# Kernel tuning notes

Measured on AMD Instinct MI355X. Metric: run time of the kernel, lower is better.

## Reference

```python
import jax, jax.numpy as jnp
import numpy as np

D = 1024
N = 4096
K = 16


def setup_inputs() -> dict:
    key = jax.random.key(0)
    ks = jax.random.split(key, 10)
    s = 1.0 / np.sqrt(3 * D)
    return {
        "token": jax.random.normal(ks[0], (N, D), jnp.float32),
        "routed_tokens": jax.random.normal(ks[1], (N, K, D), jnp.float32),
        "sim_row": jax.random.normal(ks[2], (N, K), jnp.float32),
        "delta_emb": jax.random.normal(ks[3], (N, K, D), jnp.float32),
        "W_logic": jax.random.uniform(ks[4], (3 * D, D), jnp.float32, -s, s),
        "b_logic": jax.random.uniform(ks[5], (D,), jnp.float32, -s, s),
        "ln_gamma": jnp.ones((D,), jnp.float32),
        "ln_beta": jnp.zeros((D,), jnp.float32),
        "W_gate": jax.random.uniform(ks[6], (3 * D, D), jnp.float32, -s, s),
        "b_gate": jax.random.uniform(ks[7], (D,), jnp.float32, -s, s),
    }


def _layernorm(x, gamma, beta, eps=1e-5):
    mu = jnp.mean(x, axis=-1, keepdims=True)
    var = jnp.mean(jnp.square(x - mu), axis=-1, keepdims=True)
    return (x - mu) * jax.lax.rsqrt(var + eps) * gamma + beta


def reference(token, routed_tokens, sim_row, delta_emb,
              W_logic, b_logic, ln_gamma, ln_beta, W_gate, b_gate):
    n, k, d = routed_tokens.shape
    token_exp = jnp.broadcast_to(token[:, None, :], (n, k, d))
    combined = jnp.concatenate([token_exp, routed_tokens, delta_emb], axis=-1)  # [N,K,3D]
    h = jnp.einsum('nke,ed->nkd', combined, W_logic) + b_logic
    fused = _layernorm(jax.nn.gelu(h, approximate=False), ln_gamma, ln_beta)  # [N,K,D]
    sim_w = jax.nn.softmax(sim_row, axis=-1)  # [N,K]
    arg_summary = jnp.einsum('nk,nkd->nd', sim_w, fused)  # [N,D]
    gate_in = jnp.concatenate([token, arg_summary, arg_summary], axis=-1)  # [N,3D]
    gate = jax.nn.sigmoid(gate_in @ W_gate + b_gate)  # [N,D]
    return (arg_summary, gate)
```

## Files before the change

### kernel.cpp

```cpp
#include <hip/hip_runtime.h>
#include <hip/hip_bf16.h>


typedef __attribute__((ext_vector_type(4))) float f32x4;
typedef __attribute__((ext_vector_type(8))) short bf16x8;

__device__ __forceinline__ ushort f2bf(float f) {
  unsigned b = __builtin_bit_cast(unsigned, f);
  b += 0x7FFFu + ((b >> 16) & 1u);
  return (ushort)(b >> 16);
}
__device__ __forceinline__ unsigned pk2(float a, float b) {
  return (unsigned)f2bf(a) | ((unsigned)f2bf(b) << 16);
}

__device__ __forceinline__ unsigned swz(unsigned a) {
  return a ^ (((a >> 7) & 3u) << 4);
}

__device__ __forceinline__ bf16x8 cvt8(const float* p) {
  f32x4 a = *(const f32x4*)p;
  f32x4 b = *(const f32x4*)(p + 4);
  bf16x8 r;
  r[0] = (short)f2bf(a[0]); r[1] = (short)f2bf(a[1]);
  r[2] = (short)f2bf(a[2]); r[3] = (short)f2bf(a[3]);
  r[4] = (short)f2bf(b[0]); r[5] = (short)f2bf(b[1]);
  r[6] = (short)f2bf(b[2]); r[7] = (short)f2bf(b[3]);
  return r;
}

__global__ __launch_bounds__(256) void prep_kernel(
    const float* __restrict__ Wl, const float* __restrict__ Wg,
    ushort* __restrict__ Bmain, ushort* __restrict__ Bk1,
    ushort* __restrict__ Bgate) {
  __shared__ float L[32][129];
  int t = threadIdx.x;
  int bid = blockIdx.x;
  const float* src; int row0, mode, kt, wg; ushort* dst;
  if (bid < 512)      { mode = 0; kt = bid >> 3;        wg = bid & 7; src = Wl; row0 = 1024 + kt * 32; dst = Bmain; }
  else if (bid < 768) { mode = 1; kt = (bid - 512) >> 3; wg = (bid - 512) & 7; src = Wl; row0 = kt * 32; dst = Bk1; }
  else                { mode = 2; kt = (bid - 768) >> 3; wg = (bid - 768) & 7; src = Wg; row0 = kt * 32; dst = Bgate; }
  int col0 = wg * 128;
  bool dosum = (mode == 2) && (kt >= 32);
#pragma unroll
  for (int p = 0; p < 4; ++p) {
    int r = p * 8 + (t >> 5), c = (t & 31) * 4;
    const float* sp = src + (size_t)(row0 + r) * 1024 + col0 + c;
    f32x4 v = *(const f32x4*)sp;
    if (dosum) { f32x4 v2 = *(const f32x4*)(sp + (size_t)1024 * 1024); v += v2; }
    L[r][c] = v[0]; L[r][c + 1] = v[1]; L[r][c + 2] = v[2]; L[r][c + 3] = v[3];
  }
  __syncthreads();
  if (mode == 0) {
    for (int c = t; c < 512; c += 256) {
      int nf = c >> 6, lane = c & 63, lr_ = lane & 15, lh_ = lane >> 4;
      bf16x8 o;
#pragma unroll
      for (int m = 0; m < 8; ++m) o[m] = (short)f2bf(L[lh_ * 8 + m][nf * 16 + lr_]);
      *(bf16x8*)(dst + (size_t)kt * 32768 + wg * 4096 + c * 8) = o;
    }
  } else {
    for (int c = t; c < 512; c += 256) {
      int nn = c >> 2, q = c & 3;
      bf16x8 o;
#pragma unroll
      for (int m = 0; m < 8; ++m) o[m] = (short)f2bf(L[q * 8 + m][nn]);
      *(bf16x8*)(dst + (size_t)kt * 32768 + (size_t)(wg * 128 + nn) * 32 + q * 8) = o;
    }
  }
}

template <int NKT, int NSPLIT, int ACT>
__global__ __launch_bounds__(256) void gemm_small(
    const float* __restrict__ A0, const float* __restrict__ A1,
    const ushort* __restrict__ Bp, const float* __restrict__ bias,
    float* __restrict__ Cout) {
  int tid = threadIdx.x, l = tid & 63, wid = tid >> 6;
  int wm = wid & 1, wn = wid >> 1;
  int mbase = blockIdx.x * 64 + wm * 32;
  int nbase = blockIdx.y * 128 + wn * 64;
  int lr = l & 15, lh = l >> 4;
  f32x4 acc[2][4] = {};
#pragma unroll 1
  for (int kt = 0; kt < NKT; ++kt) {
    const float* As = (kt < NSPLIT) ? A0 : A1;
    int ke = ((kt < NSPLIT) ? kt : kt - NSPLIT) * 32 + lh * 8;
    bf16x8 af[2];
#pragma unroll
    for (int mf = 0; mf < 2; ++mf)
      af[mf] = cvt8(As + (size_t)(mbase + mf * 16 + lr) * 1024 + ke);
    bf16x8 bf[4];
#pragma unroll
    for (int nf = 0; nf < 4; ++nf)
      bf[nf] = *(const bf16x8*)(Bp + (size_t)kt * 32768 +
                                (size_t)(nbase + nf * 16 + lr) * 32 + lh * 8);
#pragma unroll
    for (int nf = 0; nf < 4; ++nf)
#pragma unroll
      for (int mf = 0; mf < 2; ++mf)
        acc[mf][nf] = __builtin_amdgcn_mfma_f32_16x16x32_bf16(
            af[mf], bf[nf], acc[mf][nf], 0, 0, 0);
  }
#pragma unroll
  for (int nf = 0; nf < 4; ++nf) {
    int col = nbase + nf * 16 + lr;
    float bs = bias[col];
#pragma unroll
    for (int mf = 0; mf < 2; ++mf)
#pragma unroll
      for (int j = 0; j < 4; ++j) {
        int row = mbase + mf * 16 + lh * 4 + j;
        float v = acc[mf][nf][j] + bs;
        if (ACT == 1) v = 1.0f / (1.0f + expf(-v));
        Cout[(size_t)row * 1024 + col] = v;
      }
  }
}

#define MFMA_STEP(ABSYM, BF) do {                                         \
  const char* ab_ = (const char*)(ABSYM) + aoff0;                         \
  bf16x8 af_[4];                                                          \
  _Pragma("unroll")                                                       \
  for (int mf = 0; mf < 4; ++mf)                                          \
    af_[mf] = *(const bf16x8*)(ab_ + mf * 1024);                          \
  _Pragma("unroll")                                                       \
  for (int nf = 0; nf < 4; ++nf)                                          \
    _Pragma("unroll")                                                     \
    for (int mf = 0; mf < 4; ++mf)                                        \
      acc[mf][nf] = __builtin_amdgcn_mfma_f32_16x16x32_bf16(              \
          af_[mf], (BF)[nf], acc[mf][nf], 0, 0, 0);                       \
} while (0)

#define BARRIER_LG() do {                                                 \
  asm volatile("s_waitcnt lgkmcnt(0)" ::: "memory");                      \
  __builtin_amdgcn_s_barrier();                                           \
  asm volatile("" ::: "memory");                                          \
} while (0)

__global__ __launch_bounds__(1024) void main_kernel(
    const float* __restrict__ routed, const float* __restrict__ delta,
    const float* __restrict__ simrow, const ushort* __restrict__ Bmain,
    const float* __restrict__ tpart, const float* __restrict__ gamma,
    const float* __restrict__ beta, float* __restrict__ out_arg) {
  __shared__ ushort Ab0[2048];
  __shared__ ushort Ab1[2048];
  __shared__ float ldsW[64];
  __shared__ float lnS[64 * 16], lnQ[64 * 16];

  int tid = threadIdx.x, l = tid & 63, wid = tid >> 6;
  int bx = blockIdx.x;
  int lr = l & 15, lh = l >> 4;

  if (tid < 4) {
    int n = bx * 4 + tid;
    float sv[16], mx = -1e30f;
#pragma unroll
    for (int j = 0; j < 16; ++j) { sv[j] = simrow[n * 16 + j]; mx = fmaxf(mx, sv[j]); }
    float s = 0.f;
#pragma unroll
    for (int j = 0; j < 16; ++j) { sv[j] = expf(sv[j] - mx); s += sv[j]; }
    float inv = 1.0f / s;
#pragma unroll
    for (int j = 0; j < 16; ++j) ldsW[tid * 16 + j] = sv[j] * inv;
  }

  const int arow = tid >> 4;
  const float* rbase = routed + (size_t)(bx * 64 + arow) * 1024 + (tid & 15) * 2;
  const float* dbase = delta  + (size_t)(bx * 64 + arow) * 1024 + (tid & 15) * 2;
  const unsigned adst = swz((unsigned)tid * 4);

  const unsigned aoff0 = swz((unsigned)lr * 64 + (unsigned)lh * 16);

  const ushort* bptr = Bmain + (size_t)(wid >> 1) * 4096 +
                       (size_t)(wid & 1) * 2048 + (size_t)l * 8;

  float2 t0 = *(const float2*)rbase;
  float2 avA = *(const float2*)(rbase + 32);
  float2 avB;
  bf16x8 bfA[4], bfB[4];
#pragma unroll
  for (int nf = 0; nf < 4; ++nf)
    bfA[nf] = *(const bf16x8*)(bptr + nf * 512);
  *(unsigned*)((char*)Ab0 + adst) = pk2(t0.x, t0.y);
  BARRIER_LG();

  f32x4 acc[4][4] = {};
#pragma unroll 1
  for (int kt = 0; kt < 64; kt += 2) {
    {
      const float* as_ = (kt + 2 < 32) ? rbase : dbase;
      avB = *(const float2*)(as_ + (size_t)((kt + 2) & 31) * 32);
    }
#pragma unroll
    for (int nf = 0; nf < 4; ++nf)
      bfB[nf] = *(const bf16x8*)(bptr + 32768 + nf * 512);
    MFMA_STEP(Ab0, bfA);
    *(unsigned*)((char*)Ab1 + adst) = pk2(avA.x, avA.y);
    BARRIER_LG();
    {
      const float* as_ = (kt + 3 < 32) ? rbase : dbase;
      avA = *(const float2*)(as_ + (size_t)((kt + 3) & 31) * 32);
    }
#pragma unroll
    for (int nf = 0; nf < 4; ++nf)
      bfA[nf] = *(const bf16x8*)(bptr + 65536 + nf * 512);
    MFMA_STEP(Ab1, bfB);
    *(unsigned*)((char*)Ab0 + adst) = pk2(avB.x, avB.y);
    BARRIER_LG();
    bptr += 65536;
  }

  const float inv_d = 1.0f / 1024.0f;
  float gam[4], bet[4];
#pragma unroll
  for (int nf = 0; nf < 4; ++nf) {
    int c = wid * 64 + nf * 16 + lr;
    gam[nf] = gamma[c]; bet[nf] = beta[c];
  }
#pragma unroll
  for (int mf = 0; mf < 4; ++mf) {
    int tokrow = bx * 4 + mf;
    float s[4] = {0, 0, 0, 0}, q[4] = {0, 0, 0, 0};
#pragma unroll
    for (int nf = 0; nf < 4; ++nf) {
      float tp = tpart[(size_t)tokrow * 1024 + wid * 64 + nf * 16 + lr];
#pragma unroll
      for (int j = 0; j < 4; ++j) {
        float h = acc[mf][nf][j] + tp;
        float g = 0.5f * h * (1.0f + erff(h * 0.70710678118654752f));
        acc[mf][nf][j] = g;
        s[j] += g; q[j] += g * g;
      }
    }
#pragma unroll
    for (int j = 0; j < 4; ++j) {
#pragma unroll
      for (int d = 1; d <= 8; d <<= 1) {
        s[j] += __shfl_xor(s[j], d, 64);
        q[j] += __shfl_xor(q[j], d, 64);
      }
    }
    if (lr == 0) {
#pragma unroll
      for (int j = 0; j < 4; ++j) {
        int row = mf * 16 + lh * 4 + j;
        lnS[row * 16 + wid] = s[j];
        lnQ[row * 16 + wid] = q[j];
      }
    }
  }
  __syncthreads();
#pragma unroll
  for (int mf = 0; mf < 4; ++mf) {
    float mu[4], rs[4], wk[4];
#pragma unroll
    for (int j = 0; j < 4; ++j) {
      int row = mf * 16 + lh * 4 + j;
      float S = 0.f, Q = 0.f;
#pragma unroll
      for (int w4 = 0; w4 < 4; ++w4) {
        f32x4 vs = *(const f32x4*)&lnS[row * 16 + w4 * 4];
        f32x4 vq = *(const f32x4*)&lnQ[row * 16 + w4 * 4];
        S += vs[0] + vs[1] + vs[2] + vs[3];
        Q += vq[0] + vq[1] + vq[2] + vq[3];
      }
      float m_ = S * inv_d;
      mu[j] = m_;
      rs[j] = rsqrtf(Q * inv_d - m_ * m_ + 1e-5f);
      wk[j] = ldsW[row];
    }
#pragma unroll
    for (int nf = 0; nf < 4; ++nf) {
      float ws = 0.f;
#pragma unroll
      for (int j = 0; j < 4; ++j) {
        float y = (acc[mf][nf][j] - mu[j]) * rs[j] * gam[nf] + bet[nf];
        ws += wk[j] * y;
      }
      ws += __shfl_xor(ws, 16, 64);
      ws += __shfl_xor(ws, 32, 64);
      if (lh == 0)
        out_arg[(size_t)(bx * 4 + mf) * 1024 + wid * 64 + nf * 16 + lr] = ws;
    }
  }
}

extern "C" void kernel_launch(void* const* d_in, const int* in_sizes, int n_in,
                              void* d_out, int out_size, void* d_ws, size_t ws_size,
                              hipStream_t stream) {
  const float* token  = (const float*)d_in[0];
  const float* routed = (const float*)d_in[1];
  const float* simrow = (const float*)d_in[2];
  const float* delta  = (const float*)d_in[3];
  const float* Wl     = (const float*)d_in[4];
  const float* bl     = (const float*)d_in[5];
  const float* gamma  = (const float*)d_in[6];
  const float* beta   = (const float*)d_in[7];
  const float* Wg     = (const float*)d_in[8];
  const float* bg     = (const float*)d_in[9];

  char* ws = (char*)d_ws;
  ushort* Bmain = (ushort*)(ws);
  ushort* Bk1   = (ushort*)(ws + (4u << 20));
  ushort* Bgate = (ushort*)(ws + (6u << 20));
  float*  tpart = (float*)(ws + (10u << 20));

  float* out_arg  = (float*)d_out;
  float* out_gate = out_arg + (size_t)4096 * 1024;

  prep_kernel<<<1280, 256, 0, stream>>>(Wl, Wg, Bmain, Bk1, Bgate);
  gemm_small<32, 32, 0><<<dim3(64, 8), 256, 0, stream>>>(
      token, token, Bk1, bl, tpart);
  main_kernel<<<1024, 1024, 0, stream>>>(
      routed, delta, simrow, Bmain, tpart, gamma, beta, out_arg);
  gemm_small<64, 32, 1><<<dim3(64, 8), 256, 0, stream>>>(
      token, out_arg, Bgate, bg, out_gate);
}
```

Measured before the change: 532.7 us.

## Batch four K-steps per barrier with a double-buffered four-slot LDS ring

The main GEMM loop now stages four 32-wide K tiles of A in LDS per group, using two four-slot buffers. It issues one barrier per four MFMA steps instead of one per step. A loads are prefetched further ahead, and each A fragment is interleaved with its MFMAs to cut register pressure. This trades more LDS (32KB for A) and a deeper prefetch chain for fewer workgroup-wide synchronisations.

```diff
diff --git a/kernel.cpp b/kernel.cpp
--- a/kernel.cpp
+++ b/kernel.cpp
@@ -117,33 +117,36 @@
   }
 }
 
-#define MFMA_STEP(ABSYM, BF) do {                                         \
-  const char* ab_ = (const char*)(ABSYM) + aoff0;                         \
-  bf16x8 af_[4];                                                          \
-  _Pragma("unroll")                                                       \
-  for (int mf = 0; mf < 4; ++mf)                                          \
-    af_[mf] = *(const bf16x8*)(ab_ + mf * 1024);                          \
-  _Pragma("unroll")                                                       \
-  for (int nf = 0; nf < 4; ++nf)                                          \
-    _Pragma("unroll")                                                     \
-    for (int mf = 0; mf < 4; ++mf)                                        \
-      acc[mf][nf] = __builtin_amdgcn_mfma_f32_16x16x32_bf16(              \
-          af_[mf], (BF)[nf], acc[mf][nf], 0, 0, 0);                       \
-} while (0)
-
 #define BARRIER_LG() do {                                                 \
   asm volatile("s_waitcnt lgkmcnt(0)" ::: "memory");                      \
   __builtin_amdgcn_s_barrier();                                           \
   asm volatile("" ::: "memory");                                          \
 } while (0)
 
+#define GSTEP(J, BCONS, BLOAD, AVC, AVN) do {                             \
+  _Pragma("unroll")                                                       \
+  for (int nf = 0; nf < 4; ++nf)                                          \
+    BLOAD[nf] = *(const bf16x8*)(bptr + ((J) + 1) * 32768 + nf * 512);    \
+  { int tt = kt0 + 5 + (J);                                               \
+    const float* as_ = ((tt & 63) < 32) ? rbase : dbase;                  \
+    AVN = *(const float2*)(as_ + (size_t)(tt & 31) * 32); }               \
+  _Pragma("unroll")                                                       \
+  for (int mf = 0; mf < 4; ++mf) {                                        \
+    bf16x8 af = *(const bf16x8*)(rdB + (J) * 4096 + aoff0 + mf * 1024);   \
+    _Pragma("unroll")                                                     \
+    for (int nf = 0; nf < 4; ++nf)                                        \
+      acc[mf][nf] = __builtin_amdgcn_mfma_f32_16x16x32_bf16(              \
+          af, (BCONS)[nf], acc[mf][nf], 0, 0, 0);                         \
+  }                                                                       \
+  *(unsigned*)(wrB + (J) * 4096 + adst) = pk2((AVC).x, (AVC).y);          \
+} while (0)
+
 __global__ __launch_bounds__(1024) void main_kernel(
     const float* __restrict__ routed, const float* __restrict__ delta,
     const float* __restrict__ simrow, const ushort* __restrict__ Bmain,
     const float* __restrict__ tpart, const float* __restrict__ gamma,
     const float* __restrict__ beta, float* __restrict__ out_arg) {
-  __shared__ ushort Ab0[2048];
-  __shared__ ushort Ab1[2048];
+  __shared__ ushort AbS[2][4][2048];
   __shared__ float ldsW[64];
   __shared__ float lnS[64 * 16], lnQ[64 * 16];
 
@@ -164,9 +167,8 @@
     for (int j = 0; j < 16; ++j) ldsW[tid * 16 + j] = sv[j] * inv;
   }
 
-  const int arow = tid >> 4;
-  const float* rbase = routed + (size_t)(bx * 64 + arow) * 1024 + (tid & 15) * 2;
-  const float* dbase = delta  + (size_t)(bx * 64 + arow) * 1024 + (tid & 15) * 2;
+  const float* rbase = routed + (size_t)(bx * 64 + (tid >> 4)) * 1024 + (tid & 15) * 2;
+  const float* dbase = delta  + (size_t)(bx * 64 + (tid >> 4)) * 1024 + (tid & 15) * 2;
   const unsigned adst = swz((unsigned)tid * 4);
 
   const unsigned aoff0 = swz((unsigned)lr * 64 + (unsigned)lh * 16);
@@ -174,40 +176,32 @@
   const ushort* bptr = Bmain + (size_t)(wid >> 1) * 4096 +
                        (size_t)(wid & 1) * 2048 + (size_t)l * 8;
 
-  float2 t0 = *(const float2*)rbase;
-  float2 avA = *(const float2*)(rbase + 32);
+  char* smemA = (char*)AbS;
+#pragma unroll
+  for (int t = 0; t < 4; ++t) {
+    float2 v = *(const float2*)(rbase + t * 32);
+    *(unsigned*)(smemA + t * 4096 + adst) = pk2(v.x, v.y);
+  }
+  float2 avA = *(const float2*)(rbase + 128);
   float2 avB;
   bf16x8 bfA[4], bfB[4];
 #pragma unroll
   for (int nf = 0; nf < 4; ++nf)
     bfA[nf] = *(const bf16x8*)(bptr + nf * 512);
-  *(unsigned*)((char*)Ab0 + adst) = pk2(t0.x, t0.y);
   BARRIER_LG();
 
   f32x4 acc[4][4] = {};
 #pragma unroll 1
-  for (int kt = 0; kt < 64; kt += 2) {
-    {
-      const float* as_ = (kt + 2 < 32) ? rbase : dbase;
-      avB = *(const float2*)(as_ + (size_t)((kt + 2) & 31) * 32);
-    }
-#pragma unroll
-    for (int nf = 0; nf < 4; ++nf)
-      bfB[nf] = *(const bf16x8*)(bptr + 32768 + nf * 512);
-    MFMA_STEP(Ab0, bfA);
-    *(unsigned*)((char*)Ab1 + adst) = pk2(avA.x, avA.y);
+  for (int g = 0; g < 16; ++g) {
+    const char* rdB = smemA + ((unsigned)(g & 1) << 14);
+    char* wrB = smemA + ((unsigned)((g & 1) ^ 1) << 14);
+    const int kt0 = g * 4;
+    GSTEP(0, bfA, bfB, avA, avB);
+    GSTEP(1, bfB, bfA, avB, avA);
+    GSTEP(2, bfA, bfB, avA, avB);
+    GSTEP(3, bfB, bfA, avB, avA);
+    bptr += 4 * 32768;
     BARRIER_LG();
-    {
-      const float* as_ = (kt + 3 < 32) ? rbase : dbase;
-      avA = *(const float2*)(as_ + (size_t)((kt + 3) & 31) * 32);
-    }
-#pragma unroll
-    for (int nf = 0; nf < 4; ++nf)
-      bfA[nf] = *(const bf16x8*)(bptr + 65536 + nf * 512);
-    MFMA_STEP(Ab1, bfB);
-    *(unsigned*)((char*)Ab0 + adst) = pk2(avB.x, avB.y);
-    BARRIER_LG();
-    bptr += 65536;
   }
 
   const float inv_d = 1.0f / 1024.0f;
```

New measurement: 591.8 us. 11.1% more time.
